# Kernel tuning notes

Measured on AMD Instinct MI355X. Metric: run time of the kernel, lower is better.

The kernel has to match this reference:

```python
import jax, jax.numpy as jnp
import numpy as np

N_NODES = 100000


def setup_inputs() -> dict:
    key = jax.random.key(0)
    k1, k2, k3 = jax.random.split(key, 3)
    x = jax.random.normal(k1, (N_NODES, 128), dtype=jnp.float32)
    edge_index = jax.random.randint(k2, (2, 1600000), 0, N_NODES, dtype=jnp.int64)
    # GCNConv linear weight (hidden, input) and bias; PReLU slope (init 0.25 as in torch)
    W = jax.random.normal(k3, (128, 128), dtype=jnp.float32) * (1.0 / np.sqrt(128))
    b = jnp.zeros((128,), dtype=jnp.float32)
    prelu_a = jnp.full((1,), 0.25, dtype=jnp.float32)
    return {"x": x, "edge_index": edge_index, "W": W, "b": b, "prelu_a": prelu_a}


def reference(x, edge_index, W, b, prelu_a):
    n = x.shape[0]
    # add self loops (as in forward's add_self_loops)
    loop = jnp.arange(n, dtype=edge_index.dtype)
    src = jnp.concatenate([edge_index[0], loop])  # [E+N]
    dst = jnp.concatenate([edge_index[1], loop])
    # linear transform first (small GEMM), then gather/scatter on hidden dim
    h = x @ W.T  # [N, H]
    # symmetric degree normalization 1/sqrt(deg_src * deg_dst), deg = in-degree incl. self-loop
    ones = jnp.ones_like(dst, dtype=h.dtype)
    deg = jax.ops.segment_sum(ones, dst, num_segments=n)
    dinv = jnp.where(deg > 0, jax.lax.rsqrt(deg), 0.0)  # [N]
    norm = dinv[src] * dinv[dst]  # [E+N]
    msg = h[src] * norm[:, None]  # gather + scale, memory-bound
    out = jax.ops.segment_sum(msg, dst, num_segments=n) + b  # scatter-add
    # PReLU (single shared slope); dropout is identity in eval mode
    out = jnp.where(out >= 0, out, prelu_a[0] * out)
    return out
```

## Files before the change

### kernel.cpp

```cpp
#include <hip/hip_runtime.h>
#include <math.h>

#define HDIM 128
#define BSH 9
#define CAP 10240
#define CH 4096
#define GEMM_BLKS 256

typedef __attribute__((ext_vector_type(8))) short short8;
typedef __attribute__((ext_vector_type(4))) float f32x4;

__device__ inline unsigned short bf16_hi(float f) {
    return (unsigned short)(__float_as_uint(f) >> 16);
}
__device__ inline unsigned short bf16_rn(float f) {
    unsigned int u = __float_as_uint(f);
    return (unsigned short)((u + 0x7FFF + ((u >> 16) & 1)) >> 16);
}

__global__ __launch_bounds__(256) void prep_kernel(
    const float* __restrict__ W, uint4* __restrict__ Whg, uint4* __restrict__ Wlg,
    int* __restrict__ bcur) {
    const int t = threadIdx.x;
    bcur[t] = t * CAP;
    for (int idx = t; idx < 2048; idx += 256) {
        const int j = idx >> 4;
        const int c = idx & 15;
        const float4* wp = (const float4*)(W + (size_t)j * HDIM + c * 8);
        float4 va = wp[0], vb = wp[1];
        float vs[8] = {va.x, va.y, va.z, va.w, vb.x, vb.y, vb.z, vb.w};
        unsigned short h[8], l[8];
        #pragma unroll
        for (int k = 0; k < 8; ++k) {
            h[k] = bf16_hi(vs[k]);
            float hf = __uint_as_float((unsigned int)h[k] << 16);
            l[k] = bf16_hi(vs[k] - hf);
        }
        uint4 hch, lch;
        hch.x = (unsigned int)h[0] | ((unsigned int)h[1] << 16);
        hch.y = (unsigned int)h[2] | ((unsigned int)h[3] << 16);
        hch.z = (unsigned int)h[4] | ((unsigned int)h[5] << 16);
        hch.w = (unsigned int)h[6] | ((unsigned int)h[7] << 16);
        lch.x = (unsigned int)l[0] | ((unsigned int)l[1] << 16);
        lch.y = (unsigned int)l[2] | ((unsigned int)l[3] << 16);
        lch.z = (unsigned int)l[4] | ((unsigned int)l[5] << 16);
        lch.w = (unsigned int)l[6] | ((unsigned int)l[7] << 16);
        Whg[idx] = hch;
        Wlg[idx] = lch;
    }
}

__device__ __forceinline__ void gemm_body(
    const float* __restrict__ x, const uint4* __restrict__ Whg,
    const uint4* __restrict__ Wlg, unsigned short* __restrict__ gb, int n,
    int g0, int g1, int bid, int nblk) {
    const int t = threadIdx.x;
    const int wave = t >> 6;
    const int lane = t & 63;
    const int q = lane >> 4;
    const int m = lane & 15;

    for (int grp = g0 + bid; grp < g1; grp += nblk) {
        const int rowbase = (grp << 7) + (wave << 5);

        f32x4 acc[2][8];
        #pragma unroll
        for (int mt = 0; mt < 2; ++mt)
            #pragma unroll
            for (int ct = 0; ct < 8; ++ct)
                acc[mt][ct] = (f32x4){0.f, 0.f, 0.f, 0.f};

        #pragma unroll
        for (int kk = 0; kk < 4; ++kk) {
            short8 ah[2], al[2];
            #pragma unroll
            for (int mt = 0; mt < 2; ++mt) {
                const int r = rowbase + (mt << 4) + m;
                float vs[8];
                if (r < n) {
                    const float4* xp = (const float4*)(x + (size_t)r * HDIM + (kk << 5) + (q << 3));
                    float4 va = xp[0], vb = xp[1];
                    vs[0] = va.x; vs[1] = va.y; vs[2] = va.z; vs[3] = va.w;
                    vs[4] = vb.x; vs[5] = vb.y; vs[6] = vb.z; vs[7] = vb.w;
                } else {
                    #pragma unroll
                    for (int k = 0; k < 8; ++k) vs[k] = 0.f;
                }
                #pragma unroll
                for (int k = 0; k < 8; ++k) {
                    unsigned short h = bf16_hi(vs[k]);
                    float hf = __uint_as_float((unsigned int)h << 16);
                    unsigned short lo = bf16_hi(vs[k] - hf);
                    ah[mt][k] = (short)h;
                    al[mt][k] = (short)lo;
                }
            }
            #pragma unroll
            for (int ct = 0; ct < 8; ++ct) {
                const int nn = (ct << 4) + m;
                const int fidx = (nn << 4) | ((kk << 2) + q);
                short8 bh = *(const short8*)&Whg[fidx];
                short8 bl = *(const short8*)&Wlg[fidx];
                #pragma unroll
                for (int mt = 0; mt < 2; ++mt) {
                    acc[mt][ct] = __builtin_amdgcn_mfma_f32_16x16x32_bf16(ah[mt], bh, acc[mt][ct], 0, 0, 0);
                    acc[mt][ct] = __builtin_amdgcn_mfma_f32_16x16x32_bf16(al[mt], bh, acc[mt][ct], 0, 0, 0);
                    acc[mt][ct] = __builtin_amdgcn_mfma_f32_16x16x32_bf16(ah[mt], bl, acc[mt][ct], 0, 0, 0);
                }
            }
        }

        #pragma unroll
        for (int mt = 0; mt < 2; ++mt) {
            #pragma unroll
            for (int rr = 0; rr < 4; ++rr) {
                const int grow = rowbase + (mt << 4) + (q << 2) + rr;
                if (grow < n) {
                    unsigned short* gp = gb + (size_t)grow * HDIM + m;
                    #pragma unroll
                    for (int ct = 0; ct < 8; ++ct)
                        gp[ct << 4] = bf16_rn(acc[mt][ct][rr]);
                }
            }
        }
    }
}

__device__ __forceinline__ void binB_body(
    const int* __restrict__ ei, int E,
    int* __restrict__ bcur, unsigned int* __restrict__ eb,
    int chunk, int* hist, int* base, int* cur) {
    const int t = threadIdx.x;
    const int c0 = chunk * CH;
    hist[t] = 0;
    __syncthreads();

    int sv[CH / 256], dv[CH / 256];
    #pragma unroll
    for (int k = 0; k < CH / 256; ++k) {
        int e = c0 + t + (k << 8);
        if (e < E) {
            sv[k] = ei[e];
            dv[k] = ei[E + e];
            atomicAdd(&hist[dv[k] >> BSH], 1);
        } else {
            dv[k] = -1;
        }
    }
    __syncthreads();
    if (hist[t] > 0) base[t] = atomicAdd(&bcur[t], hist[t]);
    cur[t] = 0;
    __syncthreads();
    #pragma unroll
    for (int k = 0; k < CH / 256; ++k) {
        if (dv[k] >= 0) {
            int bkt = dv[k] >> BSH;
            int o = atomicAdd(&cur[bkt], 1);
            eb[(size_t)base[bkt] + o] =
                ((unsigned int)(dv[k] & ((1 << BSH) - 1)) << 23) | (unsigned int)sv[k];
        }
    }
}

__global__ __launch_bounds__(256) void fuseAB_kernel(
    const int* __restrict__ ei, int E, int* __restrict__ bcur,
    unsigned int* __restrict__ eb,
    const float* __restrict__ x, const uint4* __restrict__ Whg,
    const uint4* __restrict__ Wlg, unsigned short* __restrict__ gb,
    int n, int nchunk, int ngroups) {
    __shared__ int s_a[256], s_b[256], s_c[256];
    const int bid = blockIdx.x;
    if (bid < nchunk)
        binB_body(ei, E, bcur, eb, bid, s_a, s_b, s_c);
    else
        gemm_body(x, Whg, Wlg, gb, n, 0, ngroups, bid - nchunk, GEMM_BLKS);
}

__global__ __launch_bounds__(256) void scanB_kernel(
    const int* __restrict__ bcur, int* __restrict__ bbase, int NB, int E) {
    __shared__ int s[256];
    const int t = threadIdx.x;
    int v = (t < NB) ? (bcur[t] - t * CAP) : 0;
    s[t] = v;
    __syncthreads();
    for (int off = 1; off < 256; off <<= 1) {
        int u = (t >= off) ? s[t - off] : 0;
        __syncthreads();
        s[t] += u;
        __syncthreads();
    }
    int excl = s[t] - v;
    if (t < NB) bbase[t] = excl;
    if (t == 0) bbase[NB] = E;
}

__global__ __launch_bounds__(512) void binC_kernel(
    const unsigned int* __restrict__ eb, const int* __restrict__ bbase,
    int* __restrict__ row_ptr, float* __restrict__ dinv,
    int* __restrict__ col, int n) {
    __shared__ int hist[512];
    __shared__ int cur[512];
    __shared__ int wsum[8];
    const int t = threadIdx.x;
    const int b = blockIdx.x;
    const int node0 = b << BSH;
    const int o0 = bbase[b];
    const int cnt = bbase[b + 1] - o0;
    const size_t s0 = (size_t)b * CAP;

    hist[t] = 0;
    __syncthreads();
    for (int e = t; e < cnt; e += 512)
        atomicAdd(&hist[eb[s0 + e] >> 23], 1);
    __syncthreads();
    const int v = hist[t];
    int x = v;
    #pragma unroll
    for (int off = 1; off < 64; off <<= 1) {
        int u = __shfl_up(x, off);
        if ((t & 63) >= off) x += u;
    }
    if ((t & 63) == 63) wsum[t >> 6] = x;
    __syncthreads();
    if (t < 8) {
        int y = wsum[t];
        #pragma unroll
        for (int off = 1; off < 8; off <<= 1) {
            int u = __shfl_up(y, off);
            if (t >= off) y += u;
        }
        wsum[t] = y;
    }
    __syncthreads();
    int excl = x - v + ((t >> 6) ? wsum[(t >> 6) - 1] : 0);

    int node = node0 + t;
    if (node < n) {
        row_ptr[node] = o0 + excl;
        dinv[node] = rsqrtf((float)v + 1.0f);
        if (node == n - 1) row_ptr[n] = o0 + excl + v;
    }
    cur[t] = o0 + excl;
    __syncthreads();
    for (int e = t; e < cnt; e += 512) {
        unsigned int p = eb[s0 + e];
        int pos = atomicAdd(&cur[p >> 23], 1);
        col[pos] = (int)(p & 0x7FFFFF);
    }
}

#define EDGE_ACC(d, u) \
    a[0] = fmaf(d, __uint_as_float((u).x << 16), a[0]); \
    a[1] = fmaf(d, __uint_as_float((u).x & 0xffff0000u), a[1]); \
    a[2] = fmaf(d, __uint_as_float((u).y << 16), a[2]); \
    a[3] = fmaf(d, __uint_as_float((u).y & 0xffff0000u), a[3]); \
    a[4] = fmaf(d, __uint_as_float((u).z << 16), a[4]); \
    a[5] = fmaf(d, __uint_as_float((u).z & 0xffff0000u), a[5]); \
    a[6] = fmaf(d, __uint_as_float((u).w << 16), a[6]); \
    a[7] = fmaf(d, __uint_as_float((u).w & 0xffff0000u), a[7]);

__global__ __launch_bounds__(256) void gather_kernel(
    const int* __restrict__ row_ptr, const int* __restrict__ col,
    const uint4* __restrict__ gbr, const float* __restrict__ dinv,
    const float* __restrict__ bias, const float* __restrict__ prelu_a,
    float* __restrict__ out, int n) {
    const int wv = threadIdx.x >> 6;
    const int lane = threadIdx.x & 63;
    const int q = lane >> 4;
    const int l16 = lane & 15;
    const int i = blockIdx.x * 4 + wv;
    if (i >= n) return;

    const int beg = row_ptr[i];
    const int end = row_ptr[i + 1];
    const float di = dinv[i];

    float a[8];
    #pragma unroll
    for (int k = 0; k < 8; ++k) a[k] = 0.f;

    if (q == 0) {
        uint4 u = gbr[(size_t)i * 16 + l16];
        EDGE_ACC(di, u)
    }

    int e = beg + q;
    for (; e + 12 < end; e += 16) {
        int s0 = col[e];
        int s1 = col[e + 4];
        int s2 = col[e + 8];
        int s3 = col[e + 12];
        float d0 = dinv[s0], d1 = dinv[s1], d2 = dinv[s2], d3 = dinv[s3];
        uint4 u0 = gbr[(size_t)s0 * 16 + l16];
        uint4 u1 = gbr[(size_t)s1 * 16 + l16];
        uint4 u2 = gbr[(size_t)s2 * 16 + l16];
        uint4 u3 = gbr[(size_t)s3 * 16 + l16];
        EDGE_ACC(d0, u0)
        EDGE_ACC(d1, u1)
        EDGE_ACC(d2, u2)
        EDGE_ACC(d3, u3)
    }
    for (; e + 4 < end; e += 8) {
        int s0 = col[e];
        int s1 = col[e + 4];
        float d0 = dinv[s0], d1 = dinv[s1];
        uint4 u0 = gbr[(size_t)s0 * 16 + l16];
        uint4 u1 = gbr[(size_t)s1 * 16 + l16];
        EDGE_ACC(d0, u0)
        EDGE_ACC(d1, u1)
    }
    if (e < end) {
        int s = col[e];
        float d = dinv[s];
        uint4 u = gbr[(size_t)s * 16 + l16];
        EDGE_ACC(d, u)
    }

    #pragma unroll
    for (int k = 0; k < 8; ++k) {
        a[k] += __shfl_xor(a[k], 16);
        a[k] += __shfl_xor(a[k], 32);
    }

    const float aa = prelu_a[0];
    const int c0 = (l16 << 3) + (q << 1);
    float2 bb = *(const float2*)(bias + c0);
    float v0 = di * a[(q << 1) + 0] + bb.x;
    float v1 = di * a[(q << 1) + 1] + bb.y;
    v0 = v0 >= 0.f ? v0 : aa * v0;
    v1 = v1 >= 0.f ? v1 : aa * v1;
    *(float2*)(out + (size_t)i * HDIM + c0) = make_float2(v0, v1);
}

extern "C" void kernel_launch(void* const* d_in, const int* in_sizes, int n_in,
                              void* d_out, int out_size, void* d_ws, size_t ws_size,
                              hipStream_t stream) {
    const float* x  = (const float*)d_in[0];
    const int*   ei = (const int*)d_in[1];
    const float* W  = (const float*)d_in[2];
    const float* b  = (const float*)d_in[3];
    const float* pa = (const float*)d_in[4];

    const int n = in_sizes[0] / HDIM;
    const int E = in_sizes[1] / 2;
    const int NB = (n + (1 << BSH) - 1) >> BSH;
    const int ngroups = (n + 127) >> 7;

    float* out = (float*)d_out;

    unsigned short* gb      = (unsigned short*)d_ws;
    unsigned int*   eb      = (unsigned int*)(gb + (size_t)n * HDIM);
    uint4*          Whg     = (uint4*)(eb + (size_t)NB * CAP);
    uint4*          Wlg     = Whg + 2048;
    float*          dinv    = (float*)(Wlg + 2048);
    int*            row_ptr = (int*)(dinv + n);
    int*            col     = row_ptr + (n + 1);
    int*            bcur    = col + E;
    int*            bbase   = bcur + 256;

    const int nchunk = (E + CH - 1) / CH;
    prep_kernel<<<1, 256, 0, stream>>>(W, Whg, Wlg, bcur);
    fuseAB_kernel<<<nchunk + GEMM_BLKS, 256, 0, stream>>>(ei, E, bcur, eb, x, Whg, Wlg, gb, n, nchunk, ngroups);
    scanB_kernel<<<1, 256, 0, stream>>>(bcur, bbase, NB, E);
    binC_kernel<<<NB, 512, 0, stream>>>(eb, bbase, row_ptr, dinv, col, n);
    gather_kernel<<<(n + 3) / 4, 256, 0, stream>>>(row_ptr, col, (const uint4*)gb, dinv, b, pa, out, n);
}
```

Before: 237.8 us.

## Fold bucket scan into binC, cache edges in registers, shrink GEMM grid

Removes the single-block scan kernel launch: each binC block now computes its own bucket offset by reducing counts of all earlier buckets in shared memory. Bucketed edges are loaded once into a per-thread register array and reused for both the histogram and the scatter pass, instead of being read from global memory twice. The GEMM block count in the fused kernel drops from 256 to 121. In exchange, every block does a redundant prefix reduction, and the 20-entry register array raises register pressure in binC.

```diff
diff --git a/kernel.cpp b/kernel.cpp
--- a/kernel.cpp
+++ b/kernel.cpp
@@ -5,7 +5,7 @@
 #define BSH 9
 #define CAP 10240
 #define CH 4096
-#define GEMM_BLKS 256
+#define GEMM_BLKS 121
 
 typedef __attribute__((ext_vector_type(8))) short short8;
 typedef __attribute__((ext_vector_type(4))) float f32x4;
@@ -176,42 +176,43 @@
         gemm_body(x, Whg, Wlg, gb, n, 0, ngroups, bid - nchunk, GEMM_BLKS);
 }
 
-__global__ __launch_bounds__(256) void scanB_kernel(
-    const int* __restrict__ bcur, int* __restrict__ bbase, int NB, int E) {
-    __shared__ int s[256];
-    const int t = threadIdx.x;
-    int v = (t < NB) ? (bcur[t] - t * CAP) : 0;
-    s[t] = v;
-    __syncthreads();
-    for (int off = 1; off < 256; off <<= 1) {
-        int u = (t >= off) ? s[t - off] : 0;
-        __syncthreads();
-        s[t] += u;
-        __syncthreads();
-    }
-    int excl = s[t] - v;
-    if (t < NB) bbase[t] = excl;
-    if (t == 0) bbase[NB] = E;
-}
-
 __global__ __launch_bounds__(512) void binC_kernel(
-    const unsigned int* __restrict__ eb, const int* __restrict__ bbase,
+    const unsigned int* __restrict__ eb, const int* __restrict__ bcur,
     int* __restrict__ row_ptr, float* __restrict__ dinv,
-    int* __restrict__ col, int n) {
+    int* __restrict__ col, int n, int NB) {
     __shared__ int hist[512];
     __shared__ int cur[512];
+    __shared__ int red[512];
     __shared__ int wsum[8];
     const int t = threadIdx.x;
     const int b = blockIdx.x;
     const int node0 = b << BSH;
-    const int o0 = bbase[b];
-    const int cnt = bbase[b + 1] - o0;
     const size_t s0 = (size_t)b * CAP;
+    const int cnt = bcur[b] - b * CAP;
+
+    red[t] = (t < b) ? (bcur[t] - t * CAP) : 0;
+    __syncthreads();
+    #pragma unroll
+    for (int off = 256; off > 0; off >>= 1) {
+        if (t < off) red[t] += red[t + off];
+        __syncthreads();
+    }
+    const int o0 = red[0];
+
+    unsigned int r[CAP / 512];
+    #pragma unroll
+    for (int k = 0; k < CAP / 512; ++k) {
+        const int e = t + (k << 9);
+        r[k] = (e < cnt) ? eb[s0 + e] : 0u;
+    }
 
     hist[t] = 0;
     __syncthreads();
-    for (int e = t; e < cnt; e += 512)
-        atomicAdd(&hist[eb[s0 + e] >> 23], 1);
+    #pragma unroll
+    for (int k = 0; k < CAP / 512; ++k) {
+        const int e = t + (k << 9);
+        if (e < cnt) atomicAdd(&hist[r[k] >> 23], 1);
+    }
     __syncthreads();
     const int v = hist[t];
     int x = v;
@@ -242,10 +243,13 @@
     }
     cur[t] = o0 + excl;
     __syncthreads();
-    for (int e = t; e < cnt; e += 512) {
-        unsigned int p = eb[s0 + e];
-        int pos = atomicAdd(&cur[p >> 23], 1);
-        col[pos] = (int)(p & 0x7FFFFF);
+    #pragma unroll
+    for (int k = 0; k < CAP / 512; ++k) {
+        const int e = t + (k << 9);
+        if (e < cnt) {
+            int pos = atomicAdd(&cur[r[k] >> 23], 1);
+            col[pos] = (int)(r[k] & 0x7FFFFF);
+        }
     }
 }
 
@@ -356,12 +360,10 @@
     int*            row_ptr = (int*)(dinv + n);
     int*            col     = row_ptr + (n + 1);
     int*            bcur    = col + E;
-    int*            bbase   = bcur + 256;
 
     const int nchunk = (E + CH - 1) / CH;
     prep_kernel<<<1, 256, 0, stream>>>(W, Whg, Wlg, bcur);
     fuseAB_kernel<<<nchunk + GEMM_BLKS, 256, 0, stream>>>(ei, E, bcur, eb, x, Whg, Wlg, gb, n, nchunk, ngroups);
-    scanB_kernel<<<1, 256, 0, stream>>>(bcur, bbase, NB, E);
-    binC_kernel<<<NB, 512, 0, stream>>>(eb, bbase, row_ptr, dinv, col, n);
+    binC_kernel<<<NB, 512, 0, stream>>>(eb, bcur, row_ptr, dinv, col, n, NB);
     gather_kernel<<<(n + 3) / 4, 256, 0, stream>>>(row_ptr, col, (const uint4*)gb, dinv, b, pa, out, n);
 }
```

Result: slower. 252.8 us (+6.3%).
